# Optimization experiments

Measured on AMD Instinct MI355X. Metric: run time of the kernel, lower is better.

The kernel has to match this reference:

```python
import jax, jax.numpy as jnp
import numpy as np

VERTEX_W = 1.0
SMOOTH_W = 0.1
SYM_W = 0.05
CHAMFER_W = 0.1

B, N = 4, 8192  # N points per cloud, flat dim = N*3


def setup_inputs() -> dict:
    key = jax.random.key(0)
    k1, k2 = jax.random.split(key)
    pred = jax.random.normal(k1, (B, N * 3), dtype=jnp.float32)
    targ = jax.random.normal(k2, (B, N * 3), dtype=jnp.float32)
    return {"pred_vertices": pred, "target_vertices": targ}


def _chamfer(x, y):
    # x: [B,N,3], y: [B,M,3]; euclidean cdist via matmul expansion
    x2 = jnp.sum(x * x, axis=-1)  # [B,N]
    y2 = jnp.sum(y * y, axis=-1)  # [B,M]
    xy = jnp.einsum('bnd,bmd->bnm', x, y)  # [B,N,M]
    d2 = x2[:, :, None] + y2[None if False else slice(None), None, :] - 2.0 * xy
    d = jnp.sqrt(jnp.maximum(d2, 0.0))
    return jnp.mean(jnp.min(d, axis=2)) + jnp.mean(jnp.min(d, axis=1))


def reference(pred_vertices, target_vertices):
    b = pred_vertices.shape[0]
    pv = pred_vertices.reshape(b, -1, 3)
    tv = target_vertices.reshape(b, -1, 3)

    # vertex MSE (on flat tensors, same as mse on reshaped)
    vertex_loss = jnp.mean((pred_vertices - target_vertices) ** 2)

    # smoothness: mean L2 norm of consecutive vertex diffs
    diff = pv[:, 1:, :] - pv[:, :-1, :]
    smoothness_loss = jnp.mean(jnp.linalg.norm(diff, axis=2))

    # symmetry: N is even in this config
    mid = pv.shape[1] // 2
    left = pv[:, :mid, :]
    right = jnp.flip(pv[:, mid:, :], axis=1)
    right = right.at[:, :, 0].multiply(-1.0)
    symmetry_loss = jnp.mean((left - right) ** 2)

    chamfer_loss = _chamfer(pv, tv)

    total = (VERTEX_W * vertex_loss + SMOOTH_W * smoothness_loss
             + SYM_W * symmetry_loss + CHAMFER_W * chamfer_loss)
    return total
```

## Files before the change

kernel.cpp:

```cpp
#include <hip/hip_runtime.h>
#include <hip/hip_bf16.h>


#define B_ 4
#define N_ 8192
#define MID_ (N_ / 2)
#define CNT_OFF 1536
#define RP_OFF 1664
#define PM_OFF 4096
#define PACK_OFF (PM_OFF + 4 * 2 * B_ * N_)
#define PACK_STRIDE (B_ * N_ * 16)

typedef short short8 __attribute__((ext_vector_type(8)));
typedef float f32x16 __attribute__((ext_vector_type(16)));

__global__ void AdvancedLoss3D_1881195675843_kernel() {}

__device__ __forceinline__ void async16(void* lds, const void* g) {
    __builtin_amdgcn_global_load_lds(
        (const __attribute__((address_space(1))) unsigned int*)g,
        (__attribute__((address_space(3))) unsigned int*)lds,
        16, 0, 0);
}

__device__ inline unsigned short bfu(float x) {
    union { __hip_bfloat16 b; unsigned short u; } c;
    c.b = __float2bfloat16(x);
    return c.u;
}
__device__ inline float bff(unsigned short u) {
    union { __hip_bfloat16 b; unsigned short u; } c;
    c.u = u;
    return __bfloat162float(c.b);
}

__device__ inline void enc(float x, float y, float z,
                           unsigned short* A, unsigned short* Bv) {
    float n2 = fmaf(x, x, fmaf(y, y, z * z));
    unsigned short hx = bfu(x), hy = bfu(y), hz = bfu(z);
    float fx = bff(hx), fy = bff(hy), fz = bff(hz);
    unsigned short lx = bfu(x - fx), ly = bfu(y - fy), lz = bfu(z - fz);
    unsigned short mx = bfu(-2.f * fx), my = bfu(-2.f * fy), mz = bfu(-2.f * fz);
    unsigned short nx = bfu(-2.f * bff(lx)), ny = bfu(-2.f * bff(ly)),
                   nz = bfu(-2.f * bff(lz));
    unsigned short n2h = bfu(n2);
    unsigned short n2l = bfu(n2 - bff(n2h));
    unsigned short one = bfu(1.0f);
    A[0] = mx; A[1] = my; A[2] = mz;
    A[3] = mx; A[4] = my; A[5] = mz;
    A[6] = nx; A[7] = ny; A[8] = nz;
    A[9] = n2h; A[10] = n2l; A[11] = one; A[12] = one;
    A[13] = A[14] = A[15] = 0;
    Bv[0] = hx; Bv[1] = hy; Bv[2] = hz;
    Bv[3] = lx; Bv[4] = ly; Bv[5] = lz;
    Bv[6] = hx; Bv[7] = hy; Bv[8] = hz;
    Bv[9] = one; Bv[10] = one; Bv[11] = n2h; Bv[12] = n2l;
    Bv[13] = Bv[14] = Bv[15] = 0;
}

__global__ __launch_bounds__(64) void prep_aux(const float* __restrict__ pred,
                                               const float* __restrict__ targ,
                                               float* __restrict__ ws) {
    int idx = blockIdx.x * 64 + threadIdx.x;
    int b = idx >> 13;
    int i = idx & (N_ - 1);
    const float* p = pred + (size_t)idx * 3;
    const float* t = targ + (size_t)idx * 3;
    float px = p[0], py = p[1], pz = p[2];
    float tx = t[0], ty = t[1], tz = t[2];

    if (idx == 0) ((unsigned int*)ws)[CNT_OFF] = 0u;

    unsigned short* pk = (unsigned short*)(ws + PACK_OFF);
    {
        union U { unsigned short s[16]; uint4 q[2]; } ua, ub, uc, ud;
        enc(px, py, pz, ua.s, ub.s);
        enc(tx, ty, tz, uc.s, ud.s);
        uint4* ap = (uint4*)(pk + (size_t)idx * 16);
        ap[0] = ua.q[0]; ap[1] = ua.q[1];
        uint4* bp = (uint4*)(pk + PACK_STRIDE + (size_t)idx * 16);
        bp[0] = ub.q[0]; bp[1] = ub.q[1];
        uint4* at = (uint4*)(pk + 2 * PACK_STRIDE + (size_t)idx * 16);
        at[0] = uc.q[0]; at[1] = uc.q[1];
        uint4* bt = (uint4*)(pk + 3 * PACK_STRIDE + (size_t)idx * 16);
        bt[0] = ud.q[0]; bt[1] = ud.q[1];
    }

    float dx = px - tx, dy = py - ty, dz = pz - tz;
    float dv = dx * dx + dy * dy + dz * dz;

    float sm = 0.f;
    if (i < N_ - 1) {
        float ex = p[3] - px, ey = p[4] - py, ez = p[5] - pz;
        sm = sqrtf(ex * ex + ey * ey + ez * ez);
    }

    float sy = 0.f;
    if (i < MID_) {
        const float* r = pred + ((size_t)(b * N_ + (N_ - 1 - i))) * 3;
        float ax = px + r[0];
        float ay = py - r[1];
        float az = pz - r[2];
        sy = ax * ax + ay * ay + az * az;
    }

    for (int off = 32; off; off >>= 1) {
        dv += __shfl_down(dv, off, 64);
        sm += __shfl_down(sm, off, 64);
        sy += __shfl_down(sy, off, 64);
    }
    if (threadIdx.x == 0) {
        ws[3 * blockIdx.x + 0] = dv;
        ws[3 * blockIdx.x + 1] = sm;
        ws[3 * blockIdx.x + 2] = sy;
    }
}

__global__ __launch_bounds__(256, 2) void chamfer_mfma(const unsigned short* __restrict__ packs,
                                                       float* __restrict__ pm) {
    int bid = blockIdx.x;
    int chunk = bid & 31;
    int rgb = bid >> 5;
    int dir = chunk >> 4;
    int b   = (chunk >> 2) & 3;
    int cc  = chunk & 3;
    int w   = threadIdx.x >> 6;
    int l   = threadIdx.x & 63;
    int lr  = l & 31;
    int kh  = l >> 5;

    const unsigned short* Ap = packs + (dir ? 2 : 0) * PACK_STRIDE;
    const unsigned short* Bp = packs + (dir ? 1 : 3) * PACK_STRIDE;

    int rowbase = (rgb * 4 + w) * 128;
    const unsigned short* abase = Ap + ((size_t)(b * N_ + rowbase + lr)) * 16 + kh * 8;
    short8 af[4];
#pragma unroll
    for (int i = 0; i < 4; i++)
        af[i] = *(const short8*)(abase + i * 32 * 16);

    float rmin[4][16];
#pragma unroll
    for (int i = 0; i < 4; i++)
#pragma unroll
        for (int j = 0; j < 16; j++) rmin[i][j] = 3.4e38f;

    __shared__ __align__(16) unsigned char smem[65536];
    const unsigned short* bchunk = Bp + (size_t)(b * N_ + cc * 2048) * 16;
    {
        const unsigned short* src = bchunk + (size_t)(lr * 16 + kh * 8);
#pragma unroll
        for (int t = 0; t < 16; t++) {
            int tile = w * 16 + t;
            async16(smem + (size_t)tile * 1024, src + (size_t)tile * 512);
        }
    }
    __syncthreads();

    const f32x16 zero = {0.f, 0.f, 0.f, 0.f, 0.f, 0.f, 0.f, 0.f,
                         0.f, 0.f, 0.f, 0.f, 0.f, 0.f, 0.f, 0.f};
    const unsigned char* bl = smem + kh * 512 + lr * 16;
    for (int t = 0; t < 64; t += 2) {
        short8 bE = *(const short8*)(bl + (size_t)t * 1024);
        short8 bO = *(const short8*)(bl + (size_t)(t + 1) * 1024);
#pragma unroll
        for (int i = 0; i < 4; i++) {
            f32x16 aE = __builtin_amdgcn_mfma_f32_32x32x16_bf16(af[i], bE, zero, 0, 0, 0);
            f32x16 aO = __builtin_amdgcn_mfma_f32_32x32x16_bf16(af[i], bO, zero, 0, 0, 0);
#pragma unroll
            for (int j = 0; j < 16; j++)
                rmin[i][j] = fminf(fminf(rmin[i][j], aE[j]), aO[j]);
        }
    }
    __syncthreads();

    float (*sred)[128][32] = (float (*)[128][32])smem;
#pragma unroll
    for (int i = 0; i < 4; i++)
#pragma unroll
        for (int j = 0; j < 16; j++) {
            int r = i * 32 + (j & 3) + 8 * (j >> 2) + 4 * kh;
            sred[w][r][(lr + r) & 31] = rmin[i][j];
        }
    __syncthreads();
    float* orow = pm + (size_t)cc * 65536 + dir * 32768 + b * N_ + rowbase;
#pragma unroll
    for (int rr = 0; rr < 128; rr += 64) {
        int r = rr + l;
        float v = 3.4e38f;
#pragma unroll
        for (int c = 0; c < 32; c++)
            v = fminf(v, sred[w][r][(c + r) & 31]);
        orow[r] = v;
    }
}

__global__ __launch_bounds__(256) void reduce_compose(const float* __restrict__ pm,
                                                      float* __restrict__ ws,
                                                      unsigned int* __restrict__ out) {
    int bid = blockIdx.x, tid = threadIdx.x;
    int idx = bid * 256 + tid;
    float v = 3.4e38f;
#pragma unroll
    for (int s = 0; s < 4; s++)
        v = fminf(v, pm[(size_t)s * 65536 + idx]);
    float d = sqrtf(fmaxf(v, 0.f));
    for (int off = 32; off; off >>= 1) d += __shfl_down(d, off, 64);
    __shared__ float red[4];
    __shared__ int is_last;
    int lane = tid & 63, w = tid >> 6;
    if (lane == 0) red[w] = d;
    __syncthreads();
    if (tid == 0) {
        ws[RP_OFF + bid] = red[0] + red[1] + red[2] + red[3];
        __threadfence();
        unsigned old = atomicAdd((unsigned int*)ws + CNT_OFF, 1u);
        is_last = (old == 255u);
    }
    __syncthreads();
    if (!is_last) return;

    if (tid == 0) __threadfence();
    __syncthreads();
    float rp = ws[RP_OFF + tid];
    float cr = (tid < 128) ? rp : 0.f;
    float cc = (tid < 128) ? 0.f : rp;
    float dv = ws[3 * tid]     + ws[3 * (tid + 256)];
    float sm = ws[3 * tid + 1] + ws[3 * (tid + 256) + 1];
    float sy = ws[3 * tid + 2] + ws[3 * (tid + 256) + 2];
    for (int off = 32; off; off >>= 1) {
        dv += __shfl_down(dv, off, 64);
        sm += __shfl_down(sm, off, 64);
        sy += __shfl_down(sy, off, 64);
        cr += __shfl_down(cr, off, 64);
        cc += __shfl_down(cc, off, 64);
    }
    __shared__ float red5[5][4];
    if (lane == 0) { red5[0][w] = dv; red5[1][w] = sm; red5[2][w] = sy;
                     red5[3][w] = cr; red5[4][w] = cc; }
    __syncthreads();
    if (tid == 0) {
        float S[5];
#pragma unroll
        for (int q = 0; q < 5; q++)
            S[q] = red5[q][0] + red5[q][1] + red5[q][2] + red5[q][3];
        float vertex = S[0] / (float)(B_ * N_ * 3);
        float smooth = S[1] / (float)(B_ * (N_ - 1));
        float sym    = S[2] / (float)(B_ * MID_ * 3);
        float cham   = (S[3] + S[4]) / (float)(B_ * N_);
        float total  = vertex + 0.1f * smooth + 0.05f * sym + 0.1f * cham;
        union { __hip_bfloat16 b; unsigned short u; } cv;
        cv.b = __float2bfloat16(total);
        out[0] = ((unsigned int)cv.u << 16) | (unsigned int)cv.u;
    }
}

extern "C" void kernel_launch(void* const* d_in, const int* in_sizes, int n_in,
                              void* d_out, int out_size, void* d_ws, size_t ws_size,
                              hipStream_t stream) {
    (void)in_sizes; (void)n_in; (void)out_size; (void)ws_size;
    const float* pred = (const float*)d_in[0];
    const float* targ = (const float*)d_in[1];
    float* wsf = (float*)d_ws;

    prep_aux<<<dim3(512), dim3(64), 0, stream>>>(pred, targ, wsf);
    chamfer_mfma<<<dim3(512), dim3(256), 0, stream>>>(
        (const unsigned short*)(wsf + PACK_OFF), wsf + PM_OFF);
    reduce_compose<<<dim3(256), dim3(256), 0, stream>>>(
        wsf + PM_OFF, wsf, (unsigned int*)d_out);
}
```

Before: 82.42 us.

## Compute both chamfer directions from one distance matrix pass

The chamfer kernel previously evaluated the pred-to-target and target-to-pred distance matrices as two separate MFMA sweeps. It now runs a single sweep and takes both the row minima and the column minima from the same MFMA outputs, halving the matrix multiply work. Column minima are reduced in registers and across half-waves, staged in LDS, and written as per-row-group partials that the final reduce kernel folds in. This adds extra min reductions, a shuffle and LDS stores inside the inner loop, plus a larger partial buffer for the last kernel to read.

```diff
diff --git a/kernel.cpp b/kernel.cpp
--- a/kernel.cpp
+++ b/kernel.cpp
@@ -8,7 +8,8 @@
 #define CNT_OFF 1536
 #define RP_OFF 1664
 #define PM_OFF 4096
-#define PACK_OFF (PM_OFF + 4 * 2 * B_ * N_)
+#define PMC_OFF (PM_OFF + 8 * B_ * N_)
+#define PACK_OFF (PMC_OFF + 16 * B_ * N_)
 #define PACK_STRIDE (B_ * N_ * 16)
 
 typedef short short8 __attribute__((ext_vector_type(8)));
@@ -34,8 +35,19 @@
     return __bfloat162float(c.b);
 }
 
-__device__ inline void enc(float x, float y, float z,
-                           unsigned short* A, unsigned short* Bv) {
+__device__ __forceinline__ float min3f(float a, float b, float c) {
+    return fminf(fminf(a, b), c);
+}
+__device__ __forceinline__ float tree16(f32x16 v) {
+    float m0 = min3f(v[0],  v[1],  v[2]);
+    float m1 = min3f(v[3],  v[4],  v[5]);
+    float m2 = min3f(v[6],  v[7],  v[8]);
+    float m3 = min3f(v[9],  v[10], v[11]);
+    float m4 = min3f(v[12], v[13], v[14]);
+    return fminf(min3f(m0, m1, m2), min3f(m3, m4, v[15]));
+}
+
+__device__ inline void encA(float x, float y, float z, unsigned short* A) {
     float n2 = fmaf(x, x, fmaf(y, y, z * z));
     unsigned short hx = bfu(x), hy = bfu(y), hz = bfu(z);
     float fx = bff(hx), fy = bff(hy), fz = bff(hz);
@@ -51,6 +63,15 @@
     A[6] = nx; A[7] = ny; A[8] = nz;
     A[9] = n2h; A[10] = n2l; A[11] = one; A[12] = one;
     A[13] = A[14] = A[15] = 0;
+}
+__device__ inline void encB(float x, float y, float z, unsigned short* Bv) {
+    float n2 = fmaf(x, x, fmaf(y, y, z * z));
+    unsigned short hx = bfu(x), hy = bfu(y), hz = bfu(z);
+    float fx = bff(hx), fy = bff(hy), fz = bff(hz);
+    unsigned short lx = bfu(x - fx), ly = bfu(y - fy), lz = bfu(z - fz);
+    unsigned short n2h = bfu(n2);
+    unsigned short n2l = bfu(n2 - bff(n2h));
+    unsigned short one = bfu(1.0f);
     Bv[0] = hx; Bv[1] = hy; Bv[2] = hz;
     Bv[3] = lx; Bv[4] = ly; Bv[5] = lz;
     Bv[6] = hx; Bv[7] = hy; Bv[8] = hz;
@@ -73,16 +94,12 @@
 
     unsigned short* pk = (unsigned short*)(ws + PACK_OFF);
     {
-        union U { unsigned short s[16]; uint4 q[2]; } ua, ub, uc, ud;
-        enc(px, py, pz, ua.s, ub.s);
-        enc(tx, ty, tz, uc.s, ud.s);
+        union U { unsigned short s[16]; uint4 q[2]; } ua, ud;
+        encA(px, py, pz, ua.s);
+        encB(tx, ty, tz, ud.s);
         uint4* ap = (uint4*)(pk + (size_t)idx * 16);
         ap[0] = ua.q[0]; ap[1] = ua.q[1];
-        uint4* bp = (uint4*)(pk + PACK_STRIDE + (size_t)idx * 16);
-        bp[0] = ub.q[0]; bp[1] = ub.q[1];
-        uint4* at = (uint4*)(pk + 2 * PACK_STRIDE + (size_t)idx * 16);
-        at[0] = uc.q[0]; at[1] = uc.q[1];
-        uint4* bt = (uint4*)(pk + 3 * PACK_STRIDE + (size_t)idx * 16);
+        uint4* bt = (uint4*)(pk + PACK_STRIDE + (size_t)idx * 16);
         bt[0] = ud.q[0]; bt[1] = ud.q[1];
     }
 
@@ -117,20 +134,19 @@
 }
 
 __global__ __launch_bounds__(256, 2) void chamfer_mfma(const unsigned short* __restrict__ packs,
-                                                       float* __restrict__ pm) {
+                                                       float* __restrict__ ws) {
     int bid = blockIdx.x;
     int chunk = bid & 31;
     int rgb = bid >> 5;
-    int dir = chunk >> 4;
-    int b   = (chunk >> 2) & 3;
-    int cc  = chunk & 3;
+    int b   = chunk >> 3;
+    int cc  = chunk & 7;
     int w   = threadIdx.x >> 6;
     int l   = threadIdx.x & 63;
     int lr  = l & 31;
     int kh  = l >> 5;
 
-    const unsigned short* Ap = packs + (dir ? 2 : 0) * PACK_STRIDE;
-    const unsigned short* Bp = packs + (dir ? 1 : 3) * PACK_STRIDE;
+    const unsigned short* Ap = packs;
+    const unsigned short* Bp = packs + PACK_STRIDE;
 
     int rowbase = (rgb * 4 + w) * 128;
     const unsigned short* abase = Ap + ((size_t)(b * N_ + rowbase + lr)) * 16 + kh * 8;
@@ -146,12 +162,14 @@
         for (int j = 0; j < 16; j++) rmin[i][j] = 3.4e38f;
 
     __shared__ __align__(16) unsigned char smem[65536];
-    const unsigned short* bchunk = Bp + (size_t)(b * N_ + cc * 2048) * 16;
+    float (*colbuf)[1024] = (float (*)[1024])(smem + 32768);
+
+    const unsigned short* bchunk = Bp + (size_t)(b * N_ + cc * 1024) * 16;
     {
         const unsigned short* src = bchunk + (size_t)(lr * 16 + kh * 8);
 #pragma unroll
-        for (int t = 0; t < 16; t++) {
-            int tile = w * 16 + t;
+        for (int t = 0; t < 8; t++) {
+            int tile = w * 8 + t;
             async16(smem + (size_t)tile * 1024, src + (size_t)tile * 512);
         }
     }
@@ -160,16 +178,34 @@
     const f32x16 zero = {0.f, 0.f, 0.f, 0.f, 0.f, 0.f, 0.f, 0.f,
                          0.f, 0.f, 0.f, 0.f, 0.f, 0.f, 0.f, 0.f};
     const unsigned char* bl = smem + kh * 512 + lr * 16;
-    for (int t = 0; t < 64; t += 2) {
+    for (int t = 0; t < 32; t += 2) {
         short8 bE = *(const short8*)(bl + (size_t)t * 1024);
         short8 bO = *(const short8*)(bl + (size_t)(t + 1) * 1024);
+        float cmE = 3.4e38f, cmO = 3.4e38f;
 #pragma unroll
         for (int i = 0; i < 4; i++) {
             f32x16 aE = __builtin_amdgcn_mfma_f32_32x32x16_bf16(af[i], bE, zero, 0, 0, 0);
             f32x16 aO = __builtin_amdgcn_mfma_f32_32x32x16_bf16(af[i], bO, zero, 0, 0, 0);
 #pragma unroll
             for (int j = 0; j < 16; j++)
-                rmin[i][j] = fminf(fminf(rmin[i][j], aE[j]), aO[j]);
+                rmin[i][j] = min3f(rmin[i][j], aE[j], aO[j]);
+            cmE = fminf(cmE, tree16(aE));
+            cmO = fminf(cmO, tree16(aO));
+        }
+        cmE = fminf(cmE, __shfl_xor(cmE, 32, 64));
+        cmO = fminf(cmO, __shfl_xor(cmO, 32, 64));
+        colbuf[w][t * 32 + lr] = cmE;
+        colbuf[w][(t + 1) * 32 + lr] = cmO;
+    }
+    __syncthreads();
+
+    {
+        float* pmc = ws + PMC_OFF + (size_t)rgb * 32768 + b * N_ + cc * 1024;
+#pragma unroll
+        for (int c0 = 0; c0 < 1024; c0 += 256) {
+            int c = c0 + threadIdx.x;
+            pmc[c] = fminf(fminf(colbuf[0][c], colbuf[1][c]),
+                           fminf(colbuf[2][c], colbuf[3][c]));
         }
     }
     __syncthreads();
@@ -183,7 +219,7 @@
             sred[w][r][(lr + r) & 31] = rmin[i][j];
         }
     __syncthreads();
-    float* orow = pm + (size_t)cc * 65536 + dir * 32768 + b * N_ + rowbase;
+    float* orow = ws + PM_OFF + (size_t)cc * 32768 + b * N_ + rowbase;
 #pragma unroll
     for (int rr = 0; rr < 128; rr += 64) {
         int r = rr + l;
@@ -195,15 +231,24 @@
     }
 }
 
-__global__ __launch_bounds__(256) void reduce_compose(const float* __restrict__ pm,
+__global__ __launch_bounds__(256) void reduce_compose(const float* __restrict__ ws_ro,
                                                       float* __restrict__ ws,
                                                       unsigned int* __restrict__ out) {
     int bid = blockIdx.x, tid = threadIdx.x;
     int idx = bid * 256 + tid;
     float v = 3.4e38f;
-#pragma unroll
-    for (int s = 0; s < 4; s++)
-        v = fminf(v, pm[(size_t)s * 65536 + idx]);
+    if (idx < B_ * N_) {
+        const float* pmr = ws_ro + PM_OFF;
+#pragma unroll
+        for (int s = 0; s < 8; s++)
+            v = fminf(v, pmr[(size_t)s * 32768 + idx]);
+    } else {
+        int c = idx - B_ * N_;
+        const float* pmc = ws_ro + PMC_OFF;
+#pragma unroll
+        for (int s = 0; s < 16; s++)
+            v = fminf(v, pmc[(size_t)s * 32768 + c]);
+    }
     float d = sqrtf(fmaxf(v, 0.f));
     for (int off = 32; off; off >>= 1) d += __shfl_down(d, off, 64);
     __shared__ float red[4];
@@ -265,7 +310,7 @@
 
     prep_aux<<<dim3(512), dim3(64), 0, stream>>>(pred, targ, wsf);
     chamfer_mfma<<<dim3(512), dim3(256), 0, stream>>>(
-        (const unsigned short*)(wsf + PACK_OFF), wsf + PM_OFF);
+        (const unsigned short*)(wsf + PACK_OFF), wsf);
     reduce_compose<<<dim3(256), dim3(256), 0, stream>>>(
-        wsf + PM_OFF, wsf, (unsigned int*)d_out);
-}
+        wsf, wsf, (unsigned int*)d_out);
+}
```

Result: no change. 83.20 us (+0.9%).
